# Kernel tuning notes

Hardware: AMD Instinct MI355X
Metric: run time of the kernel (lower is better)

The kernel has to match this reference:

```python
import jax, jax.numpy as jnp
import numpy as np

B, N, F_IN = 8, 4096, 128
H0, H1, OUT = 64, 32, 32
DENSITY = 0.004  # avg degree ~16


def setup_inputs() -> dict:
    key = jax.random.key(0)
    ks = jax.random.split(key, 8)
    x = jax.random.normal(ks[0], (B, N, F_IN), dtype=jnp.float32)
    # sparse binary adjacency (graph structure), stored dense as the module does
    adj = (jax.random.uniform(ks[1], (B, N, N)) < DENSITY).astype(jnp.float32)
    def w(k, i, o):
        return jax.random.normal(k, (i, o), dtype=jnp.float32) * (1.0 / np.sqrt(i))
    return {
        "x": x, "adj": adj,
        "Ws0": w(ks[2], F_IN, H0), "Wn0": w(ks[3], F_IN, H0), "b0": jnp.zeros((H0,), jnp.float32),
        "Ws1": w(ks[4], H0, H1),   "Wn1": w(ks[5], H0, H1),   "b1": jnp.zeros((H1,), jnp.float32),
        "Ws2": w(ks[6], H1, OUT),  "Wn2": w(ks[7], H1, OUT),  "b2": jnp.zeros((OUT,), jnp.float32),
    }


def _sage_layer(h, adj, deg_inv, Ws, Wn, b):
    # mean over incoming neighbors: row j of adj selects messages into node j
    neigh = jnp.einsum('bij,bjd->bid', adj, h) * deg_inv  # [B,N,d_in]
    return jax.nn.relu(h @ Ws + neigh @ Wn + b)


def reference(x, adj, Ws0, Wn0, b0, Ws1, Wn1, b1, Ws2, Wn2, b2):
    deg = jnp.sum(adj, axis=-1, keepdims=True)  # [B,N,1] in-degree
    deg_inv = 1.0 / jnp.maximum(deg, 1.0)
    h = _sage_layer(x, adj, deg_inv, Ws0, Wn0, b0)
    h = _sage_layer(h, adj, deg_inv, Ws1, Wn1, b1)
    h = _sage_layer(h, adj, deg_inv, Ws2, Wn2, b2)
    # original flattens to [B*N, out_dim] embeddings
    return h.reshape(B * N, -1)
```

## Files before the change

### kernel.cpp

```cpp
#include <hip/hip_runtime.h>
#include <hip/hip_bf16.h>

#define BN      32768
#define NCOL    4096
#define MAX_NBR 64

#define WS_NBR 0
#define WS_DEG (4*1024*1024)
#define WS_H0  (WS_DEG + 131072)
#define WS_H1  (WS_H0 + 8*1024*1024)

__global__ __launch_bounds__(256) void build_csr_kernel(
    const float* __restrict__ adj,
    unsigned short* __restrict__ nbr,
    int* __restrict__ deg)
{
    __shared__ int s_cnt[4];
    __shared__ unsigned short s_list[4][MAX_NBR];
    const int wave = threadIdx.x >> 6, lane = threadIdx.x & 63;
    const int row  = (blockIdx.x << 2) + wave;
    if (lane == 0) s_cnt[wave] = 0;
    __syncthreads();

    const uint4* arow = reinterpret_cast<const uint4*>(adj + (size_t)row * NCOL);
    #pragma unroll
    for (int t = 0; t < 16; ++t) {
        const uint4 q = arow[t * 64 + lane];
        if (q.x | q.y | q.z | q.w) {
            const int c4 = (t * 64 + lane) * 4;
            if (q.x) { int p = atomicAdd(&s_cnt[wave], 1);
                       if (p < MAX_NBR) s_list[wave][p] = (unsigned short)(c4    ); }
            if (q.y) { int p = atomicAdd(&s_cnt[wave], 1);
                       if (p < MAX_NBR) s_list[wave][p] = (unsigned short)(c4 + 1); }
            if (q.z) { int p = atomicAdd(&s_cnt[wave], 1);
                       if (p < MAX_NBR) s_list[wave][p] = (unsigned short)(c4 + 2); }
            if (q.w) { int p = atomicAdd(&s_cnt[wave], 1);
                       if (p < MAX_NBR) s_list[wave][p] = (unsigned short)(c4 + 3); }
        }
    }
    __syncthreads();
    const int cnt = s_cnt[wave];
    const int cl  = cnt < MAX_NBR ? cnt : MAX_NBR;
    if (lane < cl) nbr[(size_t)row * MAX_NBR + lane] = s_list[wave][lane];
    if (lane == 0) deg[row] = cnt;
}

template<int D_IN, int D_OUT>
__global__ __launch_bounds__(256) void gather_layer_kernel(
    const float* __restrict__ hin,
    const unsigned short* __restrict__ nbr,
    const int* __restrict__ deg,
    const float* __restrict__ Ws, const float* __restrict__ Wn,
    const float* __restrict__ bias,
    float* __restrict__ hout)
{
    constexpr int SUB = (D_IN >= 64) ? 1 : (64 / D_IN);
    constexpr int KPL = (D_IN + 63) / 64;
    constexpr int NW  = 4 * SUB;
    __shared__ float s_self[D_IN];
    __shared__ float s_part[NW][D_IN];
    __shared__ float s_neigh[D_IN];

    const int tid  = threadIdx.x;
    const int wave = tid >> 6, lane = tid & 63;
    const int sub  = (D_IN < 64) ? (lane / D_IN) : 0;
    const int sl   = (D_IN < 64) ? (lane % D_IN) : lane;
    const int strm = wave * SUB + sub;
    const int row  = ((blockIdx.x & 7) << 12) | (blockIdx.x >> 3);
    const int jbase = row & ~(NCOL - 1);

    const int d   = deg[row];
    const int cnt = d < MAX_NBR ? d : MAX_NBR;
    const float dinv = 1.0f / (float)(d > 1 ? d : 1);

    int mycol = 0;
    if (lane < cnt) mycol = nbr[(size_t)row * MAX_NBR + lane];

    if (wave == 0) {
        if constexpr (KPL == 2) {
            const float2 f = *(const float2*)(hin + (size_t)row * D_IN + 2 * lane);
            s_self[2 * lane] = f.x; s_self[2 * lane + 1] = f.y;
        } else {
            if (lane < D_IN) s_self[lane] = hin[(size_t)row * D_IN + lane];
        }
    }

    float nv[KPL];
    #pragma unroll
    for (int i = 0; i < KPL; ++i) nv[i] = 0.f;
    for (int t = strm; t < cnt; t += NW) {
        const int j = jbase + __shfl(mycol, t, 64);
        if constexpr (KPL == 2) {
            const float2 f = *(const float2*)(hin + (size_t)j * D_IN + 2 * lane);
            nv[0] += f.x; nv[1] += f.y;
        } else {
            nv[0] += hin[(size_t)j * D_IN + sl];
        }
    }
    if constexpr (KPL == 2) {
        s_part[strm][2 * lane]     = nv[0];
        s_part[strm][2 * lane + 1] = nv[1];
    } else {
        s_part[strm][sl] = nv[0];
    }
    __syncthreads();

    if (tid < D_IN) {
        float s = 0.f;
        #pragma unroll
        for (int p = 0; p < NW; ++p) s += s_part[p][tid];
        s_neigh[tid] = s * dinv;
    }
    __syncthreads();

    if (wave == 0) {
        constexpr int SEG  = 64 / D_OUT;
        constexpr int KSEG = D_IN / SEG;
        const int o = lane % D_OUT, seg = lane / D_OUT;
        float acc = 0.f;
        #pragma unroll 8
        for (int kk = 0; kk < KSEG; ++kk) {
            const int k = seg * KSEG + kk;
            acc = fmaf(s_self[k],  Ws[k * D_OUT + o], acc);
            acc = fmaf(s_neigh[k], Wn[k * D_OUT + o], acc);
        }
        if constexpr (SEG == 2) acc += __shfl_xor(acc, 32, 64);
        if (seg == 0)
            hout[(size_t)row * D_OUT + o] = fmaxf(acc + bias[o], 0.f);
    }
}

extern "C" void kernel_launch(void* const* d_in, const int* in_sizes, int n_in,
                              void* d_out, int out_size, void* d_ws, size_t ws_size,
                              hipStream_t stream) {
    const float* x   = (const float*)d_in[0];
    const float* adj = (const float*)d_in[1];
    const float* Ws0 = (const float*)d_in[2]; const float* Wn0 = (const float*)d_in[3];
    const float* b0  = (const float*)d_in[4];
    const float* Ws1 = (const float*)d_in[5]; const float* Wn1 = (const float*)d_in[6];
    const float* b1  = (const float*)d_in[7];
    const float* Ws2 = (const float*)d_in[8]; const float* Wn2 = (const float*)d_in[9];
    const float* b2  = (const float*)d_in[10];

    char* ws = (char*)d_ws;
    unsigned short* nbr = (unsigned short*)(ws + WS_NBR);
    int*   deg = (int*)(ws + WS_DEG);
    float* h0  = (float*)(ws + WS_H0);
    float* h1  = (float*)(ws + WS_H1);

    build_csr_kernel<<<BN / 4, 256, 0, stream>>>(adj, nbr, deg);
    gather_layer_kernel<128, 64><<<BN, 256, 0, stream>>>(
        x,  nbr, deg, Ws0, Wn0, b0, h0);
    gather_layer_kernel<64, 32><<<BN, 256, 0, stream>>>(
        h0, nbr, deg, Ws1, Wn1, b1, h1);
    gather_layer_kernel<32, 32><<<BN, 256, 0, stream>>>(
        h1, nbr, deg, Ws2, Wn2, b2, (float*)d_out);
}
```

Before: 863.6 us.

## Fuse CSR build with layer-0 gather and transform, use nontemporal adj loads

After: 836.4 us. -3.2%, faster.

```diff
diff --git a/kernel.cpp b/kernel.cpp
--- a/kernel.cpp
+++ b/kernel.cpp
@@ -10,22 +10,33 @@
 #define WS_H0  (WS_DEG + 131072)
 #define WS_H1  (WS_H0 + 8*1024*1024)
 
-__global__ __launch_bounds__(256) void build_csr_kernel(
+typedef unsigned int u32x4 __attribute__((ext_vector_type(4)));
+
+__global__ __launch_bounds__(256) void fused_csr_layer0_kernel(
     const float* __restrict__ adj,
+    const float* __restrict__ x,
+    const float* __restrict__ Ws, const float* __restrict__ Wn,
+    const float* __restrict__ bias,
     unsigned short* __restrict__ nbr,
-    int* __restrict__ deg)
+    int* __restrict__ deg,
+    float* __restrict__ h0)
 {
     __shared__ int s_cnt[4];
     __shared__ unsigned short s_list[4][MAX_NBR];
+    __shared__ float s_self[4][128];
+    __shared__ float s_neigh[4][128];
+
     const int wave = threadIdx.x >> 6, lane = threadIdx.x & 63;
-    const int row  = (blockIdx.x << 2) + wave;
+    const int row  = (((blockIdx.x & 7) << 12) | ((blockIdx.x >> 3) << 2)) + wave;
+    const int jbase = row & ~(NCOL - 1);
+
     if (lane == 0) s_cnt[wave] = 0;
     __syncthreads();
 
-    const uint4* arow = reinterpret_cast<const uint4*>(adj + (size_t)row * NCOL);
+    const u32x4* arow = reinterpret_cast<const u32x4*>(adj + (size_t)row * NCOL);
     #pragma unroll
     for (int t = 0; t < 16; ++t) {
-        const uint4 q = arow[t * 64 + lane];
+        const u32x4 q = __builtin_nontemporal_load(&arow[t * 64 + lane]);
         if (q.x | q.y | q.z | q.w) {
             const int c4 = (t * 64 + lane) * 4;
             if (q.x) { int p = atomicAdd(&s_cnt[wave], 1);
@@ -39,10 +50,34 @@
         }
     }
     __syncthreads();
-    const int cnt = s_cnt[wave];
-    const int cl  = cnt < MAX_NBR ? cnt : MAX_NBR;
-    if (lane < cl) nbr[(size_t)row * MAX_NBR + lane] = s_list[wave][lane];
-    if (lane == 0) deg[row] = cnt;
+
+    const int d   = s_cnt[wave];
+    const int cnt = d < MAX_NBR ? d : MAX_NBR;
+    const float dinv = 1.0f / (float)(d > 1 ? d : 1);
+
+    if (lane < cnt) nbr[(size_t)row * MAX_NBR + lane] = s_list[wave][lane];
+    if (lane == 0) deg[row] = d;
+
+    const float2 sf = *(const float2*)(x + (size_t)row * 128 + 2 * lane);
+    float n0 = 0.f, n1 = 0.f;
+    for (int t = 0; t < cnt; ++t) {
+        const int j = jbase + (int)s_list[wave][t];
+        const float2 f = *(const float2*)(x + (size_t)j * 128 + 2 * lane);
+        n0 += f.x; n1 += f.y;
+    }
+    s_self[wave][2 * lane]      = sf.x;
+    s_self[wave][2 * lane + 1]  = sf.y;
+    s_neigh[wave][2 * lane]     = n0 * dinv;
+    s_neigh[wave][2 * lane + 1] = n1 * dinv;
+
+    const int o = lane;
+    float acc = 0.f;
+    #pragma unroll 8
+    for (int k = 0; k < 128; ++k) {
+        acc = fmaf(s_self[wave][k],  Ws[k * 64 + o], acc);
+        acc = fmaf(s_neigh[wave][k], Wn[k * 64 + o], acc);
+    }
+    h0[(size_t)row * 64 + o] = fmaxf(acc + bias[o], 0.f);
 }
 
 template<int D_IN, int D_OUT>
@@ -148,9 +183,8 @@
     float* h0  = (float*)(ws + WS_H0);
     float* h1  = (float*)(ws + WS_H1);
 
-    build_csr_kernel<<<BN / 4, 256, 0, stream>>>(adj, nbr, deg);
-    gather_layer_kernel<128, 64><<<BN, 256, 0, stream>>>(
-        x,  nbr, deg, Ws0, Wn0, b0, h0);
+    fused_csr_layer0_kernel<<<BN / 4, 256, 0, stream>>>(
+        adj, x, Ws0, Wn0, b0, nbr, deg, h0);
     gather_layer_kernel<64, 32><<<BN, 256, 0, stream>>>(
         h0, nbr, deg, Ws1, Wn1, b1, h1);
     gather_layer_kernel<32, 32><<<BN, 256, 0, stream>>>(
```
